# Optimization experiments

Hardware: AMD Instinct MI355X
Metric: run time of the kernel (lower is better)

The kernel has to match this reference:

```python
import jax, jax.numpy as jnp
import numpy as np

B, S, CIN, H, W, D = 8, 16, 128, 64, 64, 64


def setup_inputs() -> dict:
    key = jax.random.key(0)
    ks = jax.random.split(key, 16)
    def rn(i, shape, s=0.05):
        return jax.random.normal(ks[i], shape, dtype=jnp.float32) * s
    z = lambda *sh: jnp.zeros(sh, jnp.float32)
    return {
        "x": jax.random.normal(ks[0], (B, S, CIN, H, W), dtype=jnp.float32),
        "proj_w": rn(1, (D, CIN, 1, 1)),
        "bn_gamma": jnp.ones((D,), jnp.float32),
        "bn_beta": z(D),
        "clstm_w": rn(2, (4 * D, 2 * D, 3, 3)),
        "clstm_b": z(4 * D),
        "lq_wih": rn(3, (4 * D, D)), "lq_whh": rn(4, (4 * D, D)),
        "lq_bih": z(4 * D), "lq_bhh": z(4 * D),
        "lr_wih": rn(5, (4 * D, D)), "lr_whh": rn(6, (4 * D, D)),
        "lr_bih": z(4 * D), "lr_bhh": z(4 * D),
        "fcf_w": rn(7, (D, D)), "fcf_b": z(D),
        "fcF_w": rn(8, (D, D)), "fcF_b": z(D),
        "fcQ_w": rn(9, (D, D)), "fcQ_b": z(D),
        "fcR_w": rn(10, (D, D)), "fcR_b": z(D),
        "P_init": 0.1 * jnp.eye(D, dtype=jnp.float32),
        "fc_w": rn(11, (D, D)), "fc_b": z(D),
        "fco_w": rn(12, (1, D)), "fco_b": z(1),
        "fca_w": rn(13, (1, D)), "fca_b": z(1),
    }


def _fc(zv, w, b):
    return zv @ w.T + b


def _forward(x, proj_w, bn_gamma, bn_beta, clstm_w, clstm_b,
             lq_wih, lq_whh, lq_bih, lq_bhh, lr_wih, lr_whh, lr_bih, lr_bhh,
             fcf_w, fcf_b, fcF_w, fcF_b, fcQ_w, fcQ_b, fcR_w, fcR_b,
             P_init, fc_w, fc_b, fco_w, fco_b, fca_w, fca_b):
    Bv, Sv, C, Hv, Wv = x.shape
    Dv = P_init.shape[0]
    # 1x1 projection conv + BatchNorm2d (training-mode batch statistics)
    y = x.reshape(Bv * Sv, C, Hv, Wv)
    y = jax.lax.conv_general_dilated(y, proj_w, (1, 1), "VALID")
    mu = y.mean((0, 2, 3), keepdims=True)
    var = ((y - mu) ** 2).mean((0, 2, 3), keepdims=True)
    y = (y - mu) * jax.lax.rsqrt(var + 1e-5)
    y = y * bn_gamma[None, :, None, None] + bn_beta[None, :, None, None]
    xp = y.reshape(Bv, Sv, Dv, Hv, Wv)
    x0 = xp[:, 0]  # forward uses x[:, 0] as innovation target every step
    eye = jnp.eye(Dv, dtype=x.dtype)

    def convlstm(inp, h, c):
        zc = jax.lax.conv_general_dilated(jnp.concatenate([inp, h], axis=1), clstm_w, (1, 1), "SAME")
        zc = zc + clstm_b[None, :, None, None]
        i, f, o, g = jnp.split(zc, 4, axis=1)
        c2 = jax.nn.sigmoid(f) * c + jax.nn.sigmoid(i) * jnp.tanh(g)
        return jax.nn.sigmoid(o) * jnp.tanh(c2), c2

    def lstm_cell(zv, h, c, wih, whh, bih, bhh):  # pytorch gate order i,f,g,o
        g = zv @ wih.T + h @ whh.T + bih + bhh
        i, f, gg, o = jnp.split(g, 4, axis=-1)
        c2 = jax.nn.sigmoid(f) * c + jax.nn.sigmoid(i) * jnp.tanh(gg)
        return jax.nn.sigmoid(o) * jnp.tanh(c2), c2

    def step(carry, xs):
        y_hat, hf, cf, hQ, cQ, hR, cR, P = carry
        hf, cf = convlstm(y_hat, hf, cf)            # [B,D,H,W]
        lf = jnp.transpose(hf, (0, 2, 3, 1))        # [B,H,W,D]
        y_tick = jnp.transpose(_fc(lf, fcf_w, fcf_b), (0, 3, 1, 2))
        Fv = _fc(hf.mean((2, 3)), fcF_w, fcF_b)     # [B,D]
        FF = Fv[:, :, None] * Fv[:, None, :]        # outer product F F^T
        hQ, cQ = lstm_cell(y_tick.mean((2, 3)), hQ, cQ, lq_wih, lq_whh, lq_bih, lq_bhh)
        Qm = jnp.exp(_fc(hQ, fcQ_w, fcQ_b))[:, :, None] * eye
        hR, cR = lstm_cell(xs.mean((2, 3)), hR, cR, lr_wih, lr_whh, lr_bih, lr_bhh)
        Rm = jnp.exp(_fc(hR, fcR_w, fcR_b))[:, :, None] * eye
        P = P * FF + Qm
        K = P @ jnp.linalg.inv(P + Rm)
        IK = eye - K
        P = IK @ P @ jnp.swapaxes(IK, 1, 2) + K @ Rm @ jnp.swapaxes(K, 1, 2)
        v = x0 - y_tick
        y_hat = y_tick + jnp.einsum("bij,bjhw->bihw", K, v)
        return (y_hat, hf, cf, hQ, cQ, hR, cR, P), y_hat

    z2 = jnp.zeros((Bv, Dv, Hv, Wv), x.dtype)
    z1 = jnp.zeros((Bv, Dv), x.dtype)
    P0 = jnp.broadcast_to(P_init, (Bv, Dv, Dv))
    carry0 = (x0, z2, z2, z1, z1, z1, z1, P0)
    _, ys = jax.lax.scan(step, carry0, jnp.transpose(xp, (1, 0, 2, 3, 4)))
    feat = jnp.transpose(ys, (1, 0, 2, 3, 4)).mean((3, 4))  # [B,S,D] adaptive avgpool
    feat = jax.nn.relu(_fc(feat, fc_w, fc_b))
    offset = _fc(feat, fco_w, fco_b)
    angle = _fc(feat, fca_w, fca_b)
    return offset, angle


def reference(x, proj_w, bn_gamma, bn_beta, clstm_w, clstm_b,
              lq_wih, lq_whh, lq_bih, lq_bhh, lr_wih, lr_whh, lr_bih, lr_bhh,
              fcf_w, fcf_b, fcF_w, fcF_b, fcQ_w, fcQ_b, fcR_w, fcR_b,
              P_init, fc_w, fc_b, fco_w, fco_b, fca_w, fca_b):
    return _forward(x, proj_w, bn_gamma, bn_beta, clstm_w, clstm_b,
                    lq_wih, lq_whh, lq_bih, lq_bhh, lr_wih, lr_whh, lr_bih, lr_bhh,
                    fcf_w, fcf_b, fcF_w, fcF_b, fcQ_w, fcQ_b, fcR_w, fcR_b,
                    P_init, fc_w, fc_b, fco_w, fco_b, fca_w, fca_b)
```

## Files before the change

kernel.cpp:

```cpp
#include <hip/hip_runtime.h>
#include <math.h>


__device__ __forceinline__ float sigf(float x){ return 1.0f/(1.0f + expf(-x)); }

#define FMA4(A, W, V0, V1, V2, V3) { (A).x += (W)*(V0); (A).y += (W)*(V1); (A).z += (W)*(V2); (A).w += (W)*(V3); }

__global__ __launch_bounds__(256) void k_w3(const float* __restrict__ cw, float* __restrict__ w3){
    int idx = blockIdx.x*256 + threadIdx.x;
    if (idx < 294912){
        int ddp = idx & 127;
        int rkd = idx >> 7;
        int dh  = rkd / 1152;
        int rk  = rkd - dh*1152;
        int oc  = (ddp >> 5)*64 + dh*32 + (ddp & 31);
        w3[idx] = cw[oc*1152 + rk];
    }
}

__global__ __launch_bounds__(256) void k_proj(const float* __restrict__ x, const float* __restrict__ pw,
                                              float* __restrict__ x0raw, float* __restrict__ psum,
                                              float* __restrict__ psumsq){
    __shared__ __align__(16) float smem[8192];
    const int tile = blockIdx.x;
    const int n    = blockIdx.y;
    const int tid  = threadIdx.x;
    const int pj = tid & 63, dg = tid >> 6;

    for (int r = tid; r < 8192; r += 256){
        int c = r >> 6, d = r & 63;
        smem[r] = pw[d*128 + c];
    }
    __syncthreads();

    const int p0 = tile*256 + pj*4;
    float4 acc[16];
#pragma unroll
    for (int i=0;i<16;i++) acc[i] = make_float4(0.f,0.f,0.f,0.f);

    const float* xb = x + (((size_t)n) << 19) + p0;
    for (int c = 0; c < 128; ++c){
        float4 xv = *(const float4*)(xb + ((size_t)c << 12));
        const float4* wr = (const float4*)(smem + c*64 + dg*16);
#pragma unroll
        for (int q=0;q<4;++q){
            float4 w4 = wr[q];
            FMA4(acc[q*4+0], w4.x, xv.x, xv.y, xv.z, xv.w);
            FMA4(acc[q*4+1], w4.y, xv.x, xv.y, xv.z, xv.w);
            FMA4(acc[q*4+2], w4.z, xv.x, xv.y, xv.z, xv.w);
            FMA4(acc[q*4+3], w4.w, xv.x, xv.y, xv.z, xv.w);
        }
    }

    const int t = n & 15, b = n >> 4;
    if (t == 0){
#pragma unroll
        for (int i=0;i<16;i++){
            int dd = dg*16 + i;
            *(float4*)(x0raw + (((size_t)(b*64 + dd)) << 12) + p0) = acc[i];
        }
    }
    float ls[16], lss[16];
#pragma unroll
    for (int i=0;i<16;i++){
        float4 a = acc[i];
        ls[i]  = a.x + a.y + a.z + a.w;
        lss[i] = a.x*a.x + a.y*a.y + a.z*a.z + a.w*a.w;
    }
    __syncthreads();
#pragma unroll
    for (int i=0;i<16;i++) smem[pj*65 + dg*16 + i] = ls[i];
    __syncthreads();
    if (tid < 64){
        float s = 0.f;
        for (int p=0;p<64;p++) s += smem[p*65 + tid];
        psum[((n*16 + tile) << 6) + tid] = s;
    }
    __syncthreads();
#pragma unroll
    for (int i=0;i<16;i++) smem[pj*65 + dg*16 + i] = lss[i];
    __syncthreads();
    if (tid < 64){
        float s = 0.f;
        for (int p=0;p<64;p++) s += smem[p*65 + tid];
        psumsq[((n*16 + tile) << 6) + tid] = s;
    }
}

__global__ __launch_bounds__(64) void k_bnfinal(const float* __restrict__ psum, const float* __restrict__ psumsq,
                                                const float* __restrict__ gamma, const float* __restrict__ beta,
                                                float* __restrict__ scale, float* __restrict__ shift,
                                                float* __restrict__ xmean){
    const int d = threadIdx.x;
    double gs = 0.0, gss = 0.0;
    for (int n=0;n<128;n++){
        float s = 0.f, ss = 0.f;
        for (int tl=0;tl<16;tl++){
            s  += psum  [((n*16+tl)<<6) + d];
            ss += psumsq[((n*16+tl)<<6) + d];
        }
        gs += (double)s; gss += (double)ss;
    }
    double mu  = gs  / 524288.0;
    double var = gss / 524288.0 - mu*mu;
    double sc  = (double)gamma[d] / sqrt(var + 1e-5);
    float scf = (float)sc;
    float shf = (float)((double)beta[d] - mu*sc);
    scale[d] = scf; shift[d] = shf;
    for (int n=0;n<128;n++){
        float s = 0.f;
        for (int tl=0;tl<16;tl++) s += psum[((n*16+tl)<<6) + d];
        xmean[(n<<6) + d] = (s * (1.f/4096.f)) * scf + shf;
    }
}

__global__ __launch_bounds__(256) void k_zero(float* __restrict__ z){
    size_t i = ((size_t)blockIdx.x*256 + threadIdx.x)*4;
    *(float4*)(z + i) = make_float4(0.f,0.f,0.f,0.f);
}

__global__ __launch_bounds__(256) void k_init(const float* __restrict__ scale, const float* __restrict__ shift,
                                              float* __restrict__ x0, float* __restrict__ yhat_p,
                                              const float* __restrict__ Pinit, float* __restrict__ Pg,
                                              float* __restrict__ hQ, float* __restrict__ cQ,
                                              float* __restrict__ hR, float* __restrict__ cR){
    size_t idx = (size_t)blockIdx.x*256 + threadIdx.x;
    int d = (int)((idx >> 12) & 63);
    float v = x0[idx]*scale[d] + shift[d];
    x0[idx] = v;
    int b = (int)(idx >> 18), r = (int)((idx >> 6) & 63), xx = (int)(idx & 63);
    yhat_p[(((size_t)(b*64 + d))*66 + r + 1)*72 + xx + 4] = v;
    if (idx < 512){ hQ[idx]=0.f; cQ[idx]=0.f; hR[idx]=0.f; cR[idx]=0.f; }
    if (idx < 32768) Pg[idx] = Pinit[idx & 4095];
}

__global__ __launch_bounds__(256,4) void k_conv(const float* __restrict__ yhat_p, const float* __restrict__ hfin_p,
                                                float* __restrict__ hfout_p, float* __restrict__ cf,
                                                const float* __restrict__ w3, const float* __restrict__ cb,
                                                float* __restrict__ hfpart){
    __shared__ __align__(16) float smem[8712];
    const int IB = 4608, RED = 8448;
    const int row = blockIdx.x;
    const int dh  = blockIdx.y;
    const int b   = blockIdx.z;
    const int tid = threadIdx.x;
    const int pxq = tid & 15;
    const int ocg = tid >> 4;
    const int px0 = pxq*4;
    const int ocb = ocg*8;

    float4 acc[8];
#pragma unroll
    for (int i=0;i<8;i++) acc[i] = make_float4(0.f,0.f,0.f,0.f);

    const float4* w3c = (const float4*)(w3 + (size_t)dh*147456);

    for (int icc = 0; icc < 32; ++icc){
        __syncthreads();
        {
            const float4* wsrc = w3c + (size_t)icc*1152;
#pragma unroll
            for (int j=0;j<6;++j){
                int s = tid + j*256;
                if (s < 1152){
                    *(float4*)(smem + s*4) = wsrc[s];
                } else if (s < 1368){
                    int si  = s - 1152;
                    int icl = si / 54;
                    int rem = si - icl*54;
                    int r   = rem / 18;
                    int x4  = rem - r*18;
                    int ic  = icc*4 + icl;
                    const float* f = (ic < 64) ? yhat_p : hfin_p;
                    *(float4*)(smem + IB + si*4) =
                        *(const float4*)(f + (((size_t)(b*64 + (ic & 63)))*66 + row + r)*72 + x4*4);
                }
            }
        }
        __syncthreads();
#pragma unroll
        for (int icl = 0; icl < 4; ++icl){
            float v[3][6];
#pragma unroll
            for (int ky=0; ky<3; ++ky){
                const float* vp = smem + IB + icl*216 + ky*72 + px0;
                v[ky][0] = vp[3];
                float4 va = *(const float4*)(vp + 4);
                v[ky][1]=va.x; v[ky][2]=va.y; v[ky][3]=va.z; v[ky][4]=va.w;
                v[ky][5] = vp[8];
            }
#pragma unroll
            for (int k=0;k<9;++k){
                const int ky = k/3, kx = k - ky*3;
                const float* wr = smem + (icl*9 + k)*128 + ocb;
                float4 wa = *(const float4*)(wr);
                float4 wb4 = *(const float4*)(wr + 4);
                const float v0=v[ky][kx+0], v1=v[ky][kx+1], v2=v[ky][kx+2], v3=v[ky][kx+3];
                FMA4(acc[0], wa.x, v0,v1,v2,v3);
                FMA4(acc[1], wa.y, v0,v1,v2,v3);
                FMA4(acc[2], wa.z, v0,v1,v2,v3);
                FMA4(acc[3], wa.w, v0,v1,v2,v3);
                FMA4(acc[4], wb4.x, v0,v1,v2,v3);
                FMA4(acc[5], wb4.y, v0,v1,v2,v3);
                FMA4(acc[6], wb4.z, v0,v1,v2,v3);
                FMA4(acc[7], wb4.w, v0,v1,v2,v3);
            }
        }
    }

    __syncthreads();
#pragma unroll
    for (int o=0;o<8;++o){
        smem[(px0+0)*132 + ocb + o] = acc[o].x;
        smem[(px0+1)*132 + ocb + o] = acc[o].y;
        smem[(px0+2)*132 + ocb + o] = acc[o].z;
        smem[(px0+3)*132 + ocb + o] = acc[o].w;
    }
    __syncthreads();

    const int dl  = tid & 31;
    const int pxg = tid >> 5;
    const int dg  = dh*32 + dl;
    const float biv = cb[dg], bfv = cb[64+dg], bov = cb[128+dg], bgv = cb[192+dg];
    float hsum = 0.f;
    const size_t gidx = (((size_t)(b*64 + dg)) << 12) + row*64 + pxg*8;
    const size_t pidx = (((size_t)(b*64 + dg))*66 + row + 1)*72 + pxg*8 + 4;
#pragma unroll
    for (int h2=0; h2<2; ++h2){
        float4 c_old = *(const float4*)(cf + gidx + h2*4);
        float ca[4] = {c_old.x, c_old.y, c_old.z, c_old.w};
        float c2a[4], ha[4];
#pragma unroll
        for (int e=0;e<4;++e){
            int px = pxg*8 + h2*4 + e;
            float zi = smem[px*132 +      dl] + biv;
            float zf = smem[px*132 + 32 + dl] + bfv;
            float zo = smem[px*132 + 64 + dl] + bov;
            float zg = smem[px*132 + 96 + dl] + bgv;
            c2a[e] = sigf(zf)*ca[e] + sigf(zi)*tanhf(zg);
            ha[e]  = sigf(zo)*tanhf(c2a[e]);
            hsum  += ha[e];
        }
        float4 c2 = make_float4(c2a[0],c2a[1],c2a[2],c2a[3]);
        float4 hh = make_float4(ha[0],ha[1],ha[2],ha[3]);
        *(float4*)(cf + gidx + h2*4) = c2;
        *(float4*)(hfout_p + pidx + h2*4) = hh;
    }
    smem[RED + pxg*33 + dl] = hsum;
    __syncthreads();
    if (tid < 32){
        float s = 0.f;
#pragma unroll
        for (int q=0;q<8;q++) s += smem[RED + q*33 + tid];
        hfpart[((b*64 + row) << 6) + dh*32 + tid] = s;
    }
}

__global__ __launch_bounds__(256) void k_ytick(const float* __restrict__ hf_p, const float* __restrict__ fw,
                                               const float* __restrict__ fb, float* __restrict__ ytick,
                                               float* __restrict__ ytpart){
    __shared__ __align__(16) float wsm[4096];
    __shared__ float red[4160];
    const int tile = blockIdx.x;
    const int b    = blockIdx.y;
    const int tid  = threadIdx.x;
    const int pj = tid & 63, dg = tid >> 6;

    for (int r = tid; r < 4096; r += 256){
        int e = r >> 6, dd = r & 63;
        wsm[r] = fw[dd*64 + e];
    }
    __syncthreads();

    const int p0 = tile*256 + pj*4;
    const int r = p0 >> 6, xx = p0 & 63;
    float4 acc[16];
#pragma unroll
    for (int i=0;i<16;i++) acc[i] = make_float4(0.f,0.f,0.f,0.f);

    const float* hb = hf_p + (((size_t)(b*64))*66 + r + 1)*72 + xx + 4;
    for (int e = 0; e < 64; ++e){
        float4 hv = *(const float4*)(hb + (size_t)e*4752);
        const float4* wr = (const float4*)(wsm + e*64 + dg*16);
#pragma unroll
        for (int q=0;q<4;++q){
            float4 w4 = wr[q];
            FMA4(acc[q*4+0], w4.x, hv.x, hv.y, hv.z, hv.w);
            FMA4(acc[q*4+1], w4.y, hv.x, hv.y, hv.z, hv.w);
            FMA4(acc[q*4+2], w4.z, hv.x, hv.y, hv.z, hv.w);
            FMA4(acc[q*4+3], w4.w, hv.x, hv.y, hv.z, hv.w);
        }
    }
    float ls[16];
#pragma unroll
    for (int i=0;i<16;i++){
        int dd = dg*16 + i;
        float bv = fb[dd];
        acc[i].x += bv; acc[i].y += bv; acc[i].z += bv; acc[i].w += bv;
        *(float4*)(ytick + (((size_t)(b*64 + dd)) << 12) + p0) = acc[i];
        ls[i] = acc[i].x + acc[i].y + acc[i].z + acc[i].w;
    }
#pragma unroll
    for (int i=0;i<16;i++) red[pj*65 + dg*16 + i] = ls[i];
    __syncthreads();
    if (tid < 64){
        float s = 0.f;
        for (int p=0;p<64;p++) s += red[p*65 + tid];
        ytpart[((b*16 + tile) << 6) + tid] = s;
    }
}

__global__ __launch_bounds__(256) void k_small(int t,
        const float* __restrict__ hfpart, const float* __restrict__ ytpart, const float* __restrict__ xmean,
        const float* __restrict__ fcF_w, const float* __restrict__ fcF_b,
        const float* __restrict__ lq_wih, const float* __restrict__ lq_whh,
        const float* __restrict__ lq_bih, const float* __restrict__ lq_bhh,
        const float* __restrict__ lr_wih, const float* __restrict__ lr_whh,
        const float* __restrict__ lr_bih, const float* __restrict__ lr_bhh,
        const float* __restrict__ fcQ_w, const float* __restrict__ fcQ_b,
        const float* __restrict__ fcR_w, const float* __restrict__ fcR_b,
        float* __restrict__ hQ, float* __restrict__ cQ, float* __restrict__ hR, float* __restrict__ cR,
        float* __restrict__ Pg, float* __restrict__ Kg){
    const int b = blockIdx.x, tid = threadIdx.x;
    __shared__ __align__(16) float aug[64*132];
    __shared__ __align__(16) float Pl[4096];
    __shared__ float hfm[64], ytm[64], xm[64], Fv[64], Qd[64], Rd[64], rds[64];
    __shared__ float hq_s[64], cq_s[64], hr_s[64], cr_s[64];
    __shared__ float gq[256], gr[256];

    if (tid < 64){
        float s = 0.f;
        for (int r=0;r<64;r++) s += hfpart[((b*64 + r) << 6) + tid];
        hfm[tid] = s * (1.f/4096.f);
        float s2 = 0.f;
        for (int r=0;r<16;r++) s2 += ytpart[((b*16 + r) << 6) + tid];
        ytm[tid] = s2 * (1.f/4096.f);
        xm[tid] = xmean[((b*16 + t) << 6) + tid];
        hq_s[tid] = hQ[b*64+tid]; cq_s[tid] = cQ[b*64+tid];
        hr_s[tid] = hR[b*64+tid]; cr_s[tid] = cR[b*64+tid];
    }
    __syncthreads();
    {
        int j = tid;
        float aq = lq_bih[j] + lq_bhh[j];
        float ar = lr_bih[j] + lr_bhh[j];
        for (int e=0;e<64;e++){
            aq += lq_wih[j*64+e]*ytm[e] + lq_whh[j*64+e]*hq_s[e];
            ar += lr_wih[j*64+e]*xm[e]  + lr_whh[j*64+e]*hr_s[e];
        }
        gq[j] = aq; gr[j] = ar;
    }
    if (tid < 64){
        float a = fcF_b[tid];
        for (int e=0;e<64;e++) a += fcF_w[tid*64+e]*hfm[e];
        Fv[tid] = a;
    }
    __syncthreads();
    if (tid < 64){
        int dd = tid;
        float gi = gq[dd], gf = gq[64+dd], gg = gq[128+dd], go = gq[192+dd];
        float c2 = sigf(gf)*cq_s[dd] + sigf(gi)*tanhf(gg);
        float h2 = sigf(go)*tanhf(c2);
        cq_s[dd] = c2; hq_s[dd] = h2;
        gi = gr[dd]; gf = gr[64+dd]; gg = gr[128+dd]; go = gr[192+dd];
        c2 = sigf(gf)*cr_s[dd] + sigf(gi)*tanhf(gg);
        h2 = sigf(go)*tanhf(c2);
        cr_s[dd] = c2; hr_s[dd] = h2;
    }
    __syncthreads();
    if (tid < 64){
        float aq_ = fcQ_b[tid], ar_ = fcR_b[tid];
        for (int e=0;e<64;e++){ aq_ += fcQ_w[tid*64+e]*hq_s[e]; ar_ += fcR_w[tid*64+e]*hr_s[e]; }
        Qd[tid] = expf(aq_); Rd[tid] = expf(ar_);
        hQ[b*64+tid] = hq_s[tid]; cQ[b*64+tid] = cq_s[tid];
        hR[b*64+tid] = hr_s[tid]; cR[b*64+tid] = cr_s[tid];
    }
    __syncthreads();
    for (int r = tid; r < 4096; r += 256){
        int i = r >> 6, j = r & 63;
        float p = Pg[((size_t)b << 12) + r] * Fv[i]*Fv[j] + (i==j ? Qd[i] : 0.f);
        Pl[r] = p;
        aug[i*132 + 64 + j] = p;
        aug[i*132 + j]      = p + (i==j ? Rd[i] : 0.f);
    }
    __syncthreads();
    const int r_ = tid & 63, cq_ = tid >> 6;
    for (int k = 0; k < 64; ++k){
        float akk = aug[k*132 + k];
        float f = aug[r_*132 + k] / akk;
        if (r_ != k){
#pragma unroll
            for (int u = 0; u < 8; ++u){
                int c4 = cq_*32 + u*4;
                if (c4 + 3 > k){
                    float4 pv = *(const float4*)(aug + k*132 + c4);
                    float4 av = *(const float4*)(aug + r_*132 + c4);
                    av.x = (c4+0 > k) ? av.x - f*pv.x : av.x;
                    av.y = (c4+1 > k) ? av.y - f*pv.y : av.y;
                    av.z = (c4+2 > k) ? av.z - f*pv.z : av.z;
                    av.w = (c4+3 > k) ? av.w - f*pv.w : av.w;
                    *(float4*)(aug + r_*132 + c4) = av;
                }
            }
        }
        __syncthreads();
    }
    if (tid < 64) rds[tid] = 1.0f / aug[tid*132 + tid];
    __syncthreads();
    {
        const int i = tid >> 2, jq = tid & 3;
        float4 tv[4];
#pragma unroll
        for (int q=0;q<4;++q) tv[q] = *(const float4*)(Pl + i*64 + jq*16 + q*4);
        for (int m=0;m<64;++m){
            float kim = aug[m*132 + 64 + i] * rds[m];
#pragma unroll
            for (int q=0;q<4;++q){
                float4 pv = *(const float4*)(Pl + m*64 + jq*16 + q*4);
                tv[q].x -= kim*pv.x; tv[q].y -= kim*pv.y; tv[q].z -= kim*pv.z; tv[q].w -= kim*pv.w;
            }
        }
#pragma unroll
        for (int q=0;q<4;++q) *(float4*)(aug + i*132 + jq*16 + q*4) = tv[q];
    }
    __syncthreads();
    {
        const int i = tid >> 2, jq = tid & 3;
        float4 a2[4];
#pragma unroll
        for (int q=0;q<4;++q) a2[q] = *(const float4*)(aug + i*132 + jq*16 + q*4);
        for (int m=0;m<64;++m){
            float t1im = aug[i*132 + m];
            float kim  = aug[m*132 + 64 + i] * rds[m];
            float coef = rds[m] * (kim * Rd[m] - t1im);
#pragma unroll
            for (int q=0;q<4;++q){
                float4 yv = *(const float4*)(aug + m*132 + 64 + jq*16 + q*4);
                a2[q].x += coef*yv.x; a2[q].y += coef*yv.y; a2[q].z += coef*yv.z; a2[q].w += coef*yv.w;
            }
        }
        size_t base = ((size_t)b << 12) + (size_t)i*64;
#pragma unroll
        for (int q=0;q<4;++q) *(float4*)(Pg + base + jq*16 + q*4) = a2[q];
#pragma unroll
        for (int q=0;q<4;++q){
#pragma unroll
            for (int e=0;e<4;++e){
                int j = jq*16 + q*4 + e;
                Kg[base + j] = aug[j*132 + 64 + i] * rds[j];
            }
        }
    }
}

__global__ __launch_bounds__(256) void k_apply(int t, const float* __restrict__ ytick,
                                               const float* __restrict__ x0, const float* __restrict__ Kg,
                                               float* __restrict__ yhat_p, float* __restrict__ featpart){
    __shared__ __align__(16) float kt[4096];
    __shared__ float red[4160];
    const int tile = blockIdx.x;
    const int b    = blockIdx.y;
    const int tid  = threadIdx.x;
    const int pj = tid & 63, dg = tid >> 6;

    for (int r = tid; r < 4096; r += 256){
        int i = r >> 6, j = r & 63;
        kt[j*64 + i] = Kg[((size_t)b << 12) + r];
    }
    __syncthreads();

    const int p0 = tile*256 + pj*4;
    const int r = p0 >> 6, xx = p0 & 63;
    float4 acc[16];
#pragma unroll
    for (int i=0;i<16;i++) acc[i] = make_float4(0.f,0.f,0.f,0.f);

    for (int j = 0; j < 64; ++j){
        size_t gi = (((size_t)(b*64 + j)) << 12) + p0;
        float4 xv = *(const float4*)(x0 + gi);
        float4 yv = *(const float4*)(ytick + gi);
        float u0 = xv.x - yv.x, u1 = xv.y - yv.y, u2 = xv.z - yv.z, u3 = xv.w - yv.w;
        const float4* wr = (const float4*)(kt + j*64 + dg*16);
#pragma unroll
        for (int q=0;q<4;++q){
            float4 k4 = wr[q];
            FMA4(acc[q*4+0], k4.x, u0,u1,u2,u3);
            FMA4(acc[q*4+1], k4.y, u0,u1,u2,u3);
            FMA4(acc[q*4+2], k4.z, u0,u1,u2,u3);
            FMA4(acc[q*4+3], k4.w, u0,u1,u2,u3);
        }
    }
    float ls[16];
#pragma unroll
    for (int i=0;i<16;i++){
        int dd = dg*16 + i;
        size_t gi = (((size_t)(b*64 + dd)) << 12) + p0;
        float4 yv = *(const float4*)(ytick + gi);
        float4 o;
        o.x = yv.x + acc[i].x; o.y = yv.y + acc[i].y; o.z = yv.z + acc[i].z; o.w = yv.w + acc[i].w;
        *(float4*)(yhat_p + (((size_t)(b*64 + dd))*66 + r + 1)*72 + xx + 4) = o;
        ls[i] = o.x + o.y + o.z + o.w;
    }
#pragma unroll
    for (int i=0;i<16;i++) red[pj*65 + dg*16 + i] = ls[i];
    __syncthreads();
    if (tid < 64){
        float s = 0.f;
        for (int p=0;p<64;p++) s += red[p*65 + tid];
        featpart[(((size_t)((t*8 + b)*16 + tile)) << 6) + tid] = s;
    }
}

__global__ __launch_bounds__(64) void k_head(const float* __restrict__ featpart,
                                             const float* __restrict__ fc_w, const float* __restrict__ fc_b,
                                             const float* __restrict__ fco_w, const float* __restrict__ fco_b,
                                             const float* __restrict__ fca_w, const float* __restrict__ fca_b,
                                             float* __restrict__ out){
    const int bt = blockIdx.x;
    const int b = bt >> 4, t = bt & 15;
    __shared__ float fs[64];
    const int i = threadIdx.x;
    float s = 0.f;
    for (int tile=0;tile<16;tile++) s += featpart[(((size_t)((t*8 + b)*16 + tile)) << 6) + i];
    fs[i] = s * (1.f/4096.f);
    __syncthreads();
    float a = fc_b[i];
    for (int e=0;e<64;e++) a += fc_w[i*64+e]*fs[e];
    a = fmaxf(a, 0.f);
    float po = a * fco_w[i];
    float pa = a * fca_w[i];
    for (int off=32; off; off >>= 1){ po += __shfl_down(po, off); pa += __shfl_down(pa, off); }
    if (i == 0){
        out[bt]       = po + fco_b[0];
        out[128 + bt] = pa + fca_b[0];
    }
}

extern "C" void kernel_launch(void* const* d_in, const int* in_sizes, int n_in,
                              void* d_out, int out_size, void* d_ws, size_t ws_size,
                              hipStream_t stream){
    const float* x       = (const float*)d_in[0];
    const float* proj_w  = (const float*)d_in[1];
    const float* bn_g    = (const float*)d_in[2];
    const float* bn_b    = (const float*)d_in[3];
    const float* clstm_w = (const float*)d_in[4];
    const float* clstm_b = (const float*)d_in[5];
    const float* lq_wih  = (const float*)d_in[6];
    const float* lq_whh  = (const float*)d_in[7];
    const float* lq_bih  = (const float*)d_in[8];
    const float* lq_bhh  = (const float*)d_in[9];
    const float* lr_wih  = (const float*)d_in[10];
    const float* lr_whh  = (const float*)d_in[11];
    const float* lr_bih  = (const float*)d_in[12];
    const float* lr_bhh  = (const float*)d_in[13];
    const float* fcf_w   = (const float*)d_in[14];
    const float* fcf_b   = (const float*)d_in[15];
    const float* fcF_w   = (const float*)d_in[16];
    const float* fcF_b   = (const float*)d_in[17];
    const float* fcQ_w   = (const float*)d_in[18];
    const float* fcQ_b   = (const float*)d_in[19];
    const float* fcR_w   = (const float*)d_in[20];
    const float* fcR_b   = (const float*)d_in[21];
    const float* P_init  = (const float*)d_in[22];
    const float* fc_w    = (const float*)d_in[23];
    const float* fc_b    = (const float*)d_in[24];
    const float* fco_w   = (const float*)d_in[25];
    const float* fco_b   = (const float*)d_in[26];
    const float* fca_w   = (const float*)d_in[27];
    const float* fca_b   = (const float*)d_in[28];
    float* out = (float*)d_out;
    float* ws  = (float*)d_ws;

    const size_t PF    = 2433024;
    const size_t FIELD = 2097152;
    float* yhat_p = ws;
    float* hfA_p  = ws + PF;
    float* hfB_p  = ws + 2*PF;
    float* cf     = ws + 3*PF;
    float* x0     = cf + FIELD;
    float* ytick  = x0 + FIELD;
    float* w3     = ytick + FIELD;
    float* psum   = w3 + 294912;
    float* psumsq = psum + 131072;
    float* scale  = psumsq + 131072;
    float* shift  = scale + 64;
    float* xmean  = shift + 64;
    float* hfpart = xmean + 8192;
    float* ytpart = hfpart + 32768;
    float* featpart = ytpart + 8192;
    float* hQ     = featpart + 131072;
    float* cQ     = hQ + 512;
    float* hR     = cQ + 512;
    float* cR     = hR + 512;
    float* Pg     = cR + 512;
    float* Kg     = Pg + 32768;

    hipLaunchKernelGGL(k_w3, dim3(1152), dim3(256), 0, stream, clstm_w, w3);
    hipLaunchKernelGGL(k_proj, dim3(16,128), dim3(256), 0, stream, x, proj_w, x0, psum, psumsq);
    hipLaunchKernelGGL(k_bnfinal, dim3(1), dim3(64), 0, stream, psum, psumsq, bn_g, bn_b, scale, shift, xmean);
    hipLaunchKernelGGL(k_zero, dim3(9176), dim3(256), 0, stream, ws);
    hipLaunchKernelGGL(k_init, dim3(8192), dim3(256), 0, stream, scale, shift, x0, yhat_p, P_init, Pg, hQ, cQ, hR, cR);

    for (int t = 0; t < 16; ++t){
        float* hf_in  = (t & 1) ? hfB_p : hfA_p;
        float* hf_out = (t & 1) ? hfA_p : hfB_p;
        hipLaunchKernelGGL(k_conv, dim3(64,2,8), dim3(256), 0, stream,
                           yhat_p, hf_in, hf_out, cf, w3, clstm_b, hfpart);
        hipLaunchKernelGGL(k_ytick, dim3(16,8), dim3(256), 0, stream,
                           hf_out, fcf_w, fcf_b, ytick, ytpart);
        hipLaunchKernelGGL(k_small, dim3(8), dim3(256), 0, stream, t,
                           hfpart, ytpart, xmean, fcF_w, fcF_b,
                           lq_wih, lq_whh, lq_bih, lq_bhh,
                           lr_wih, lr_whh, lr_bih, lr_bhh,
                           fcQ_w, fcQ_b, fcR_w, fcR_b,
                           hQ, cQ, hR, cR, Pg, Kg);
        hipLaunchKernelGGL(k_apply, dim3(16,8), dim3(256), 0, stream, t,
                           ytick, x0, Kg, yhat_p, featpart);
    }
    hipLaunchKernelGGL(k_head, dim3(128), dim3(64), 0, stream,
                       featpart, fc_w, fc_b, fco_w, fco_b, fca_w, fca_b, out);
}
```

Baseline: 6.530 ms.

## Fuse fcf 1x1 projection into ConvLSTM kernel with full-channel tiles and double buffering

```diff
diff --git a/kernel.cpp b/kernel.cpp
--- a/kernel.cpp
+++ b/kernel.cpp
@@ -9,11 +9,11 @@
 __global__ __launch_bounds__(256) void k_w3(const float* __restrict__ cw, float* __restrict__ w3){
     int idx = blockIdx.x*256 + threadIdx.x;
     if (idx < 294912){
-        int ddp = idx & 127;
-        int rkd = idx >> 7;
-        int dh  = rkd / 1152;
-        int rk  = rkd - dh*1152;
-        int oc  = (ddp >> 5)*64 + dh*32 + (ddp & 31);
+        int col = idx & 255;
+        int rk  = idx >> 8;
+        int ocg = col >> 3, j = col & 7;
+        int g = j >> 1, e = j & 1;
+        int oc = g*64 + ocg*2 + e;
         w3[idx] = cw[oc*1152 + rk];
     }
 }
@@ -134,184 +134,171 @@
     if (idx < 32768) Pg[idx] = Pinit[idx & 4095];
 }
 
-__global__ __launch_bounds__(256,4) void k_conv(const float* __restrict__ yhat_p, const float* __restrict__ hfin_p,
+__global__ __launch_bounds__(256,2) void k_conv(const float* __restrict__ yhat_p, const float* __restrict__ hfin_p,
                                                 float* __restrict__ hfout_p, float* __restrict__ cf,
                                                 const float* __restrict__ w3, const float* __restrict__ cb,
-                                                float* __restrict__ hfpart){
-    __shared__ __align__(16) float smem[8712];
-    const int IB = 4608, RED = 8448;
+                                                const float* __restrict__ fcf_w, const float* __restrict__ fcf_b,
+                                                float* __restrict__ ytick,
+                                                float* __restrict__ hfpart, float* __restrict__ ytpartR){
+    __shared__ __align__(16) float smem[10080];
+    const int BUF = 5040, HS = 4352, REDZ = 8704;
     const int row = blockIdx.x;
-    const int dh  = blockIdx.y;
-    const int b   = blockIdx.z;
+    const int b   = blockIdx.y;
     const int tid = threadIdx.x;
-    const int pxq = tid & 15;
-    const int ocg = tid >> 4;
-    const int px0 = pxq*4;
-    const int ocb = ocg*8;
-
-    float4 acc[8];
-#pragma unroll
-    for (int i=0;i<8;i++) acc[i] = make_float4(0.f,0.f,0.f,0.f);
-
-    const float4* w3c = (const float4*)(w3 + (size_t)dh*147456);
-
-    for (int icc = 0; icc < 32; ++icc){
-        __syncthreads();
-        {
-            const float4* wsrc = w3c + (size_t)icc*1152;
-#pragma unroll
-            for (int j=0;j<6;++j){
-                int s = tid + j*256;
-                if (s < 1152){
-                    *(float4*)(smem + s*4) = wsrc[s];
-                } else if (s < 1368){
-                    int si  = s - 1152;
-                    int icl = si / 54;
-                    int rem = si - icl*54;
-                    int r   = rem / 18;
-                    int x4  = rem - r*18;
-                    int ic  = icc*4 + icl;
-                    const float* f = (ic < 64) ? yhat_p : hfin_p;
-                    *(float4*)(smem + IB + si*4) =
-                        *(const float4*)(f + (((size_t)(b*64 + (ic & 63)))*66 + row + r)*72 + x4*4);
-                }
-            }
-        }
-        __syncthreads();
-#pragma unroll
-        for (int icl = 0; icl < 4; ++icl){
-            float v[3][6];
-#pragma unroll
-            for (int ky=0; ky<3; ++ky){
-                const float* vp = smem + IB + icl*216 + ky*72 + px0;
+    const int pxg = tid & 7;
+    const int ocg = tid >> 3;
+    const int px0 = pxg*8;
+
+    float4 acc4[16];
+#pragma unroll
+    for (int i=0;i<16;i++) acc4[i] = make_float4(0.f,0.f,0.f,0.f);
+
+    float4 st[5];
+    auto issue = [&](int icc){
+#pragma unroll
+        for (int j=0;j<5;++j){
+            int s = tid + j*256;
+            if (s < 1152){
+                st[j] = ((const float4*)w3)[(size_t)icc*1152 + s];
+            } else if (s < 1260){
+                int si = s - 1152;
+                int icl = si/54, rem = si - icl*54, r = rem/18, x4 = rem - r*18;
+                int ic  = icc*2 + icl;
+                const float* f = (ic < 64) ? yhat_p : hfin_p;
+                st[j] = *(const float4*)(f + (((size_t)(b*64 + (ic & 63)))*66 + row + r)*72 + x4*4);
+            }
+        }
+    };
+    auto commit = [&](int buf){
+#pragma unroll
+        for (int j=0;j<5;++j){
+            int s = tid + j*256;
+            if (s < 1260) *(float4*)(smem + buf*BUF + s*4) = st[j];
+        }
+    };
+
+    issue(0); commit(0); __syncthreads();
+    int p = 0;
+    for (int icc = 0; icc < 64; ++icc){
+        if (icc < 63){
+            issue(icc+1);
+        } else {
+#pragma unroll
+            for (int j=0;j<4;++j) st[j] = ((const float4*)fcf_w)[tid + j*256];
+        }
+        const float* wb = smem + p*BUF;
+        const float* ib = wb + 4608;
+#pragma unroll
+        for (int icl=0; icl<2; ++icl){
+            float v[3][10];
+#pragma unroll
+            for (int ky=0;ky<3;++ky){
+                const float* vp = ib + icl*216 + ky*72 + px0;
                 v[ky][0] = vp[3];
-                float4 va = *(const float4*)(vp + 4);
+                float4 va = *(const float4*)(vp+4);
+                float4 vb = *(const float4*)(vp+8);
                 v[ky][1]=va.x; v[ky][2]=va.y; v[ky][3]=va.z; v[ky][4]=va.w;
-                v[ky][5] = vp[8];
+                v[ky][5]=vb.x; v[ky][6]=vb.y; v[ky][7]=vb.z; v[ky][8]=vb.w;
+                v[ky][9] = vp[12];
             }
 #pragma unroll
             for (int k=0;k<9;++k){
                 const int ky = k/3, kx = k - ky*3;
-                const float* wr = smem + (icl*9 + k)*128 + ocb;
-                float4 wa = *(const float4*)(wr);
-                float4 wb4 = *(const float4*)(wr + 4);
-                const float v0=v[ky][kx+0], v1=v[ky][kx+1], v2=v[ky][kx+2], v3=v[ky][kx+3];
-                FMA4(acc[0], wa.x, v0,v1,v2,v3);
-                FMA4(acc[1], wa.y, v0,v1,v2,v3);
-                FMA4(acc[2], wa.z, v0,v1,v2,v3);
-                FMA4(acc[3], wa.w, v0,v1,v2,v3);
-                FMA4(acc[4], wb4.x, v0,v1,v2,v3);
-                FMA4(acc[5], wb4.y, v0,v1,v2,v3);
-                FMA4(acc[6], wb4.z, v0,v1,v2,v3);
-                FMA4(acc[7], wb4.w, v0,v1,v2,v3);
-            }
-        }
-    }
-
-    __syncthreads();
-#pragma unroll
-    for (int o=0;o<8;++o){
-        smem[(px0+0)*132 + ocb + o] = acc[o].x;
-        smem[(px0+1)*132 + ocb + o] = acc[o].y;
-        smem[(px0+2)*132 + ocb + o] = acc[o].z;
-        smem[(px0+3)*132 + ocb + o] = acc[o].w;
-    }
-    __syncthreads();
-
-    const int dl  = tid & 31;
-    const int pxg = tid >> 5;
-    const int dg  = dh*32 + dl;
-    const float biv = cb[dg], bfv = cb[64+dg], bov = cb[128+dg], bgv = cb[192+dg];
-    float hsum = 0.f;
-    const size_t gidx = (((size_t)(b*64 + dg)) << 12) + row*64 + pxg*8;
-    const size_t pidx = (((size_t)(b*64 + dg))*66 + row + 1)*72 + pxg*8 + 4;
-#pragma unroll
-    for (int h2=0; h2<2; ++h2){
-        float4 c_old = *(const float4*)(cf + gidx + h2*4);
-        float ca[4] = {c_old.x, c_old.y, c_old.z, c_old.w};
-        float c2a[4], ha[4];
-#pragma unroll
-        for (int e=0;e<4;++e){
-            int px = pxg*8 + h2*4 + e;
-            float zi = smem[px*132 +      dl] + biv;
-            float zf = smem[px*132 + 32 + dl] + bfv;
-            float zo = smem[px*132 + 64 + dl] + bov;
-            float zg = smem[px*132 + 96 + dl] + bgv;
-            c2a[e] = sigf(zf)*ca[e] + sigf(zi)*tanhf(zg);
-            ha[e]  = sigf(zo)*tanhf(c2a[e]);
-            hsum  += ha[e];
-        }
-        float4 c2 = make_float4(c2a[0],c2a[1],c2a[2],c2a[3]);
-        float4 hh = make_float4(ha[0],ha[1],ha[2],ha[3]);
-        *(float4*)(cf + gidx + h2*4) = c2;
-        *(float4*)(hfout_p + pidx + h2*4) = hh;
-    }
-    smem[RED + pxg*33 + dl] = hsum;
-    __syncthreads();
-    if (tid < 32){
+                const float* wr = wb + (icl*9+k)*256 + ocg*8;
+                float4 wa  = *(const float4*)(wr);
+                float4 wb4 = *(const float4*)(wr+4);
+                const float u0=v[ky][kx+0], u1=v[ky][kx+1], u2=v[ky][kx+2], u3=v[ky][kx+3];
+                const float u4=v[ky][kx+4], u5=v[ky][kx+5], u6=v[ky][kx+6], u7=v[ky][kx+7];
+                FMA4(acc4[0],  wa.x,  u0,u1,u2,u3);  FMA4(acc4[1],  wa.x,  u4,u5,u6,u7);
+                FMA4(acc4[2],  wa.y,  u0,u1,u2,u3);  FMA4(acc4[3],  wa.y,  u4,u5,u6,u7);
+                FMA4(acc4[4],  wa.z,  u0,u1,u2,u3);  FMA4(acc4[5],  wa.z,  u4,u5,u6,u7);
+                FMA4(acc4[6],  wa.w,  u0,u1,u2,u3);  FMA4(acc4[7],  wa.w,  u4,u5,u6,u7);
+                FMA4(acc4[8],  wb4.x, u0,u1,u2,u3);  FMA4(acc4[9],  wb4.x, u4,u5,u6,u7);
+                FMA4(acc4[10], wb4.y, u0,u1,u2,u3);  FMA4(acc4[11], wb4.y, u4,u5,u6,u7);
+                FMA4(acc4[12], wb4.z, u0,u1,u2,u3);  FMA4(acc4[13], wb4.z, u4,u5,u6,u7);
+                FMA4(acc4[14], wb4.w, u0,u1,u2,u3);  FMA4(acc4[15], wb4.w, u4,u5,u6,u7);
+            }
+        }
+        if (icc < 63){
+            commit(p^1);
+        } else {
+#pragma unroll
+            for (int j=0;j<4;++j){
+                int s = tid + j*256;
+                int dp = s >> 4, c4 = s & 15;
+                *(float4*)(smem + dp*68 + c4*4) = st[j];
+            }
+        }
+        __syncthreads();
+        p ^= 1;
+    }
+
+#pragma unroll
+    for (int e2=0;e2<2;++e2){
+        const int d = ocg*2 + e2;
+        const float biv = cb[d], bfv = cb[64+d], bov = cb[128+d], bgv = cb[192+d];
+        const size_t gidx = (((size_t)(b*64 + d)) << 12) + row*64 + px0;
+        const size_t pidx = (((size_t)(b*64 + d))*66 + row + 1)*72 + px0 + 4;
+#pragma unroll
+        for (int h2=0;h2<2;++h2){
+            float4 zi = acc4[(0+e2)*2 + h2];
+            float4 zf = acc4[(2+e2)*2 + h2];
+            float4 zo = acc4[(4+e2)*2 + h2];
+            float4 zg = acc4[(6+e2)*2 + h2];
+            float4 c_old = *(const float4*)(cf + gidx + h2*4);
+            float4 c2, hh;
+            c2.x = sigf(zf.x+bfv)*c_old.x + sigf(zi.x+biv)*tanhf(zg.x+bgv); hh.x = sigf(zo.x+bov)*tanhf(c2.x);
+            c2.y = sigf(zf.y+bfv)*c_old.y + sigf(zi.y+biv)*tanhf(zg.y+bgv); hh.y = sigf(zo.y+bov)*tanhf(c2.y);
+            c2.z = sigf(zf.z+bfv)*c_old.z + sigf(zi.z+biv)*tanhf(zg.z+bgv); hh.z = sigf(zo.z+bov)*tanhf(c2.z);
+            c2.w = sigf(zf.w+bfv)*c_old.w + sigf(zi.w+biv)*tanhf(zg.w+bgv); hh.w = sigf(zo.w+bov)*tanhf(c2.w);
+            *(float4*)(cf + gidx + h2*4) = c2;
+            *(float4*)(hfout_p + pidx + h2*4) = hh;
+            *(float4*)(smem + HS + d*68 + px0 + h2*4) = hh;
+        }
+    }
+    __syncthreads();
+
+    const int d0 = ocg*2;
+    float4 yt[4];
+    {
+        float b0 = fcf_b[d0], b1 = fcf_b[d0+1];
+        yt[0] = make_float4(b0,b0,b0,b0); yt[1] = yt[0];
+        yt[2] = make_float4(b1,b1,b1,b1); yt[3] = yt[2];
+    }
+    for (int d=0; d<64; ++d){
+        float4 h0 = *(const float4*)(smem + HS + d*68 + px0);
+        float4 h1 = *(const float4*)(smem + HS + d*68 + px0 + 4);
+        float w0 = smem[(d0  )*68 + d];
+        float w1 = smem[(d0+1)*68 + d];
+        FMA4(yt[0], w0, h0.x,h0.y,h0.z,h0.w);
+        FMA4(yt[1], w0, h1.x,h1.y,h1.z,h1.w);
+        FMA4(yt[2], w1, h0.x,h0.y,h0.z,h0.w);
+        FMA4(yt[3], w1, h1.x,h1.y,h1.z,h1.w);
+    }
+#pragma unroll
+    for (int e2=0;e2<2;++e2){
+        const int dp = d0 + e2;
+        size_t yi = (((size_t)(b*64 + dp)) << 12) + row*64 + px0;
+        *(float4*)(ytick + yi)     = yt[e2*2+0];
+        *(float4*)(ytick + yi + 4) = yt[e2*2+1];
+        float4 a = yt[e2*2], c = yt[e2*2+1];
+        smem[REDZ + dp*9 + pxg] = a.x+a.y+a.z+a.w + c.x+c.y+c.z+c.w;
+    }
+    __syncthreads();
+    if (tid < 64){
         float s = 0.f;
-#pragma unroll
-        for (int q=0;q<8;q++) s += smem[RED + q*33 + tid];
-        hfpart[((b*64 + row) << 6) + dh*32 + tid] = s;
-    }
-}
-
-__global__ __launch_bounds__(256) void k_ytick(const float* __restrict__ hf_p, const float* __restrict__ fw,
-                                               const float* __restrict__ fb, float* __restrict__ ytick,
-                                               float* __restrict__ ytpart){
-    __shared__ __align__(16) float wsm[4096];
-    __shared__ float red[4160];
-    const int tile = blockIdx.x;
-    const int b    = blockIdx.y;
-    const int tid  = threadIdx.x;
-    const int pj = tid & 63, dg = tid >> 6;
-
-    for (int r = tid; r < 4096; r += 256){
-        int e = r >> 6, dd = r & 63;
-        wsm[r] = fw[dd*64 + e];
-    }
-    __syncthreads();
-
-    const int p0 = tile*256 + pj*4;
-    const int r = p0 >> 6, xx = p0 & 63;
-    float4 acc[16];
-#pragma unroll
-    for (int i=0;i<16;i++) acc[i] = make_float4(0.f,0.f,0.f,0.f);
-
-    const float* hb = hf_p + (((size_t)(b*64))*66 + r + 1)*72 + xx + 4;
-    for (int e = 0; e < 64; ++e){
-        float4 hv = *(const float4*)(hb + (size_t)e*4752);
-        const float4* wr = (const float4*)(wsm + e*64 + dg*16);
-#pragma unroll
-        for (int q=0;q<4;++q){
-            float4 w4 = wr[q];
-            FMA4(acc[q*4+0], w4.x, hv.x, hv.y, hv.z, hv.w);
-            FMA4(acc[q*4+1], w4.y, hv.x, hv.y, hv.z, hv.w);
-            FMA4(acc[q*4+2], w4.z, hv.x, hv.y, hv.z, hv.w);
-            FMA4(acc[q*4+3], w4.w, hv.x, hv.y, hv.z, hv.w);
-        }
-    }
-    float ls[16];
-#pragma unroll
-    for (int i=0;i<16;i++){
-        int dd = dg*16 + i;
-        float bv = fb[dd];
-        acc[i].x += bv; acc[i].y += bv; acc[i].z += bv; acc[i].w += bv;
-        *(float4*)(ytick + (((size_t)(b*64 + dd)) << 12) + p0) = acc[i];
-        ls[i] = acc[i].x + acc[i].y + acc[i].z + acc[i].w;
-    }
-#pragma unroll
-    for (int i=0;i<16;i++) red[pj*65 + dg*16 + i] = ls[i];
-    __syncthreads();
-    if (tid < 64){
-        float s = 0.f;
-        for (int p=0;p<64;p++) s += red[p*65 + tid];
-        ytpart[((b*16 + tile) << 6) + tid] = s;
+#pragma unroll 8
+        for (int px=0;px<64;++px) s += smem[HS + tid*68 + px];
+        hfpart[((b*64 + row) << 6) + tid] = s;
+        float s2 = 0.f;
+#pragma unroll
+        for (int q=0;q<8;++q) s2 += smem[REDZ + tid*9 + q];
+        ytpartR[((b*64 + row) << 6) + tid] = s2;
     }
 }
 
 __global__ __launch_bounds__(256) void k_small(int t,
-        const float* __restrict__ hfpart, const float* __restrict__ ytpart, const float* __restrict__ xmean,
+        const float* __restrict__ hfpart, const float* __restrict__ ytpartR, const float* __restrict__ xmean,
         const float* __restrict__ fcF_w, const float* __restrict__ fcF_b,
         const float* __restrict__ lq_wih, const float* __restrict__ lq_whh,
         const float* __restrict__ lq_bih, const float* __restrict__ lq_bhh,
@@ -333,7 +320,7 @@
         for (int r=0;r<64;r++) s += hfpart[((b*64 + r) << 6) + tid];
         hfm[tid] = s * (1.f/4096.f);
         float s2 = 0.f;
-        for (int r=0;r<16;r++) s2 += ytpart[((b*16 + r) << 6) + tid];
+        for (int r=0;r<64;r++) s2 += ytpartR[((b*64 + r) << 6) + tid];
         ytm[tid] = s2 * (1.f/4096.f);
         xm[tid] = xmean[((b*16 + t) << 6) + tid];
         hq_s[tid] = hQ[b*64+tid]; cq_s[tid] = cQ[b*64+tid];
@@ -456,58 +443,55 @@
 __global__ __launch_bounds__(256) void k_apply(int t, const float* __restrict__ ytick,
                                                const float* __restrict__ x0, const float* __restrict__ Kg,
                                                float* __restrict__ yhat_p, float* __restrict__ featpart){
-    __shared__ __align__(16) float kt[4096];
-    __shared__ float red[4160];
+    __shared__ __align__(16) float kt[4160];
     const int tile = blockIdx.x;
     const int b    = blockIdx.y;
     const int tid  = threadIdx.x;
-    const int pj = tid & 63, dg = tid >> 6;
+    const int pj = tid & 31, dgp = tid >> 5;
 
     for (int r = tid; r < 4096; r += 256){
         int i = r >> 6, j = r & 63;
-        kt[j*64 + i] = Kg[((size_t)b << 12) + r];
-    }
-    __syncthreads();
-
-    const int p0 = tile*256 + pj*4;
-    const int r = p0 >> 6, xx = p0 & 63;
-    float4 acc[16];
-#pragma unroll
-    for (int i=0;i<16;i++) acc[i] = make_float4(0.f,0.f,0.f,0.f);
+        kt[j*65 + i] = Kg[((size_t)b << 12) + r];
+    }
+    __syncthreads();
+
+    const int p0 = tile*128 + pj*4;
+    const int rr = p0 >> 6, xx = p0 & 63;
+    float4 acc[8];
+#pragma unroll
+    for (int i=0;i<8;i++) acc[i] = make_float4(0.f,0.f,0.f,0.f);
 
     for (int j = 0; j < 64; ++j){
         size_t gi = (((size_t)(b*64 + j)) << 12) + p0;
         float4 xv = *(const float4*)(x0 + gi);
         float4 yv = *(const float4*)(ytick + gi);
         float u0 = xv.x - yv.x, u1 = xv.y - yv.y, u2 = xv.z - yv.z, u3 = xv.w - yv.w;
-        const float4* wr = (const float4*)(kt + j*64 + dg*16);
-#pragma unroll
-        for (int q=0;q<4;++q){
-            float4 k4 = wr[q];
-            FMA4(acc[q*4+0], k4.x, u0,u1,u2,u3);
-            FMA4(acc[q*4+1], k4.y, u0,u1,u2,u3);
-            FMA4(acc[q*4+2], k4.z, u0,u1,u2,u3);
-            FMA4(acc[q*4+3], k4.w, u0,u1,u2,u3);
-        }
-    }
-    float ls[16];
-#pragma unroll
-    for (int i=0;i<16;i++){
-        int dd = dg*16 + i;
-        size_t gi = (((size_t)(b*64 + dd)) << 12) + p0;
+        const float* kr = kt + j*65 + dgp*8;
+#pragma unroll
+        for (int il=0; il<8; ++il){
+            float kv = kr[il];
+            FMA4(acc[il], kv, u0,u1,u2,u3);
+        }
+    }
+    float ls[8];
+#pragma unroll
+    for (int il=0;il<8;++il){
+        int d = dgp*8 + il;
+        size_t gi = (((size_t)(b*64 + d)) << 12) + p0;
         float4 yv = *(const float4*)(ytick + gi);
         float4 o;
-        o.x = yv.x + acc[i].x; o.y = yv.y + acc[i].y; o.z = yv.z + acc[i].z; o.w = yv.w + acc[i].w;
-        *(float4*)(yhat_p + (((size_t)(b*64 + dd))*66 + r + 1)*72 + xx + 4) = o;
-        ls[i] = o.x + o.y + o.z + o.w;
-    }
-#pragma unroll
-    for (int i=0;i<16;i++) red[pj*65 + dg*16 + i] = ls[i];
+        o.x = yv.x + acc[il].x; o.y = yv.y + acc[il].y; o.z = yv.z + acc[il].z; o.w = yv.w + acc[il].w;
+        *(float4*)(yhat_p + (((size_t)(b*64 + d))*66 + rr + 1)*72 + xx + 4) = o;
+        ls[il] = o.x + o.y + o.z + o.w;
+    }
+    __syncthreads();
+#pragma unroll
+    for (int il=0;il<8;++il) kt[pj*65 + dgp*8 + il] = ls[il];
     __syncthreads();
     if (tid < 64){
         float s = 0.f;
-        for (int p=0;p<64;p++) s += red[p*65 + tid];
-        featpart[(((size_t)((t*8 + b)*16 + tile)) << 6) + tid] = s;
+        for (int q=0;q<32;++q) s += kt[q*65 + tid];
+        featpart[(((size_t)((t*8 + b)*32 + tile)) << 6) + tid] = s;
     }
 }
 
@@ -521,7 +505,7 @@
     __shared__ float fs[64];
     const int i = threadIdx.x;
     float s = 0.f;
-    for (int tile=0;tile<16;tile++) s += featpart[(((size_t)((t*8 + b)*16 + tile)) << 6) + i];
+    for (int tile=0;tile<32;tile++) s += featpart[(((size_t)((t*8 + b)*32 + tile)) << 6) + i];
     fs[i] = s * (1.f/4096.f);
     __syncthreads();
     float a = fc_b[i];
@@ -586,9 +570,9 @@
     float* shift  = scale + 64;
     float* xmean  = shift + 64;
     float* hfpart = xmean + 8192;
-    float* ytpart = hfpart + 32768;
-    float* featpart = ytpart + 8192;
-    float* hQ     = featpart + 131072;
+    float* ytpartR= hfpart + 32768;
+    float* featpart = ytpartR + 32768;
+    float* hQ     = featpart + 262144;
     float* cQ     = hQ + 512;
     float* hR     = cQ + 512;
     float* cR     = hR + 512;
@@ -604,17 +588,16 @@
     for (int t = 0; t < 16; ++t){
         float* hf_in  = (t & 1) ? hfB_p : hfA_p;
         float* hf_out = (t & 1) ? hfA_p : hfB_p;
-        hipLaunchKernelGGL(k_conv, dim3(64,2,8), dim3(256), 0, stream,
-                           yhat_p, hf_in, hf_out, cf, w3, clstm_b, hfpart);
-        hipLaunchKernelGGL(k_ytick, dim3(16,8), dim3(256), 0, stream,
-                           hf_out, fcf_w, fcf_b, ytick, ytpart);
+        hipLaunchKernelGGL(k_conv, dim3(64,8), dim3(256), 0, stream,
+                           yhat_p, hf_in, hf_out, cf, w3, clstm_b,
+                           fcf_w, fcf_b, ytick, hfpart, ytpartR);
         hipLaunchKernelGGL(k_small, dim3(8), dim3(256), 0, stream, t,
-                           hfpart, ytpart, xmean, fcF_w, fcF_b,
+                           hfpart, ytpartR, xmean, fcF_w, fcF_b,
                            lq_wih, lq_whh, lq_bih, lq_bhh,
                            lr_wih, lr_whh, lr_bih, lr_bhh,
                            fcQ_w, fcQ_b, fcR_w, fcR_b,
                            hQ, cQ, hR, cR, Pg, Kg);
-        hipLaunchKernelGGL(k_apply, dim3(16,8), dim3(256), 0, stream, t,
+        hipLaunchKernelGGL(k_apply, dim3(32,8), dim3(256), 0, stream, t,
                            ytick, x0, Kg, yhat_p, featpart);
     }
     hipLaunchKernelGGL(k_head, dim3(128), dim3(64), 0, stream,
```

Measured after the change: 11.54 ms. 1.77x slower.
